# Performance work log

Measured on AMD Instinct MI355X. Metric: run time of the kernel, lower is better.

The kernel has to match this reference:

```python
import jax, jax.numpy as jnp
import numpy as np

EMBED_DIM = 1024
NUM_HEADS = 16
NUM_KV_HEADS = 4
HEAD_DIM = 64
WINDOW_SIZE = 32
TOKENS_PER_FRAME = 64
BASE_T, BASE_D, BASE_B = 10000.0, 100.0, 100.0


def apply_3d_rope(x, pos_t, pos_d, pos_b):
    # x: (B, S, H, D); pos_*: (S,) int
    D = x.shape[-1]
    half = D // 2
    dim_idx = jnp.arange(half, dtype=jnp.float32)
    inv_freq = 1.0 / (BASE_T ** (2.0 * dim_idx / D))  # (half,)
    ang = (pos_t.astype(jnp.float32)[:, None] * inv_freq
           + pos_d.astype(jnp.float32)[:, None] * inv_freq * (BASE_T / BASE_D)
           + pos_b.astype(jnp.float32)[:, None] * inv_freq * (BASE_T / BASE_B))  # (S, half)
    cos = jnp.cos(ang)[None, :, None, :]
    sin = jnp.sin(ang)[None, :, None, :]
    x1 = x[..., 0::2]
    x2 = x[..., 1::2]
    y1 = x1 * cos - x2 * sin
    y2 = x1 * sin + x2 * cos
    return jnp.stack([y1, y2], axis=-1).reshape(x.shape)


def setup_inputs() -> dict:
    key = jax.random.key(0)
    ks = jax.random.split(key, 8)
    B, Sn, Lp = 1, 1024, 4096
    hidden_states = jax.random.normal(ks[0], (B, Sn, EMBED_DIM), dtype=jnp.float32)
    past_k = jax.random.normal(ks[1], (B, NUM_KV_HEADS, Lp, HEAD_DIM), dtype=jnp.float32)
    past_v = jax.random.normal(ks[2], (B, NUM_KV_HEADS, Lp, HEAD_DIM), dtype=jnp.float32)
    wq = jax.random.normal(ks[3], (EMBED_DIM, NUM_HEADS * HEAD_DIM), dtype=jnp.float32) * 0.02
    wk = jax.random.normal(ks[4], (EMBED_DIM, NUM_KV_HEADS * HEAD_DIM), dtype=jnp.float32) * 0.02
    wv = jax.random.normal(ks[5], (EMBED_DIM, NUM_KV_HEADS * HEAD_DIM), dtype=jnp.float32) * 0.02
    wo = jax.random.normal(ks[6], (NUM_HEADS * HEAD_DIM, EMBED_DIM), dtype=jnp.float32) * 0.02
    # frame-time positions: tokens_per_frame tokens share a frame time; past frames 0..63, new frames 64..79
    past_idx = jnp.arange(Lp, dtype=jnp.int32)
    new_idx = jnp.arange(Sn, dtype=jnp.int32)
    past_t = past_idx // TOKENS_PER_FRAME
    new_t = new_idx // TOKENS_PER_FRAME + Lp // TOKENS_PER_FRAME
    # 8x8 depth-by-bearing patch grid within each frame
    past_d = (past_idx % TOKENS_PER_FRAME) // 8
    past_b = past_idx % 8
    new_d = (new_idx % TOKENS_PER_FRAME) // 8
    new_b = new_idx % 8
    return dict(hidden_states=hidden_states, past_k=past_k, past_v=past_v,
                wq=wq, wk=wk, wv=wv, wo=wo,
                new_t=new_t, new_d=new_d, new_b=new_b,
                past_t=past_t, past_d=past_d, past_b=past_b)


def reference(hidden_states, past_k, past_v, wq, wk, wv, wo,
              new_t, new_d, new_b, past_t, past_d, past_b):
    B, Sn, _ = hidden_states.shape
    Lp = past_t.shape[0]
    Q = (hidden_states @ wq).reshape(B, Sn, NUM_HEADS, HEAD_DIM)
    Kn = (hidden_states @ wk).reshape(B, Sn, NUM_KV_HEADS, HEAD_DIM)
    Vn = (hidden_states @ wv).reshape(B, Sn, NUM_KV_HEADS, HEAD_DIM)
    Q = apply_3d_rope(Q, new_t, new_d, new_b)
    Kn = apply_3d_rope(Kn, new_t, new_d, new_b)
    Q = Q.transpose(0, 2, 1, 3)   # (B, H, Sn, D)
    Kn = Kn.transpose(0, 2, 1, 3)  # (B, KVH, Sn, D)
    Vn = Vn.transpose(0, 2, 1, 3)
    # Sliding-window truncation on frame time: torch does searchsorted + slice
    # (drop past keys with time < min_time). Masking those keys to -inf is
    # mathematically identical and jit-friendly (static shapes).
    min_time = new_t.max() - (WINDOW_SIZE - 1)
    past_keep = past_t >= min_time                                    # (Lp,)
    valid = jnp.concatenate([past_keep, jnp.ones((Sn,), dtype=bool)])  # (Lp+Sn,)
    pos_t = jnp.concatenate([past_t, new_t])
    K = jnp.concatenate([past_k, Kn], axis=2)  # (B, KVH, Lp+Sn, D)
    V = jnp.concatenate([past_v, Vn], axis=2)
    rep = NUM_HEADS // NUM_KV_HEADS
    K = jnp.repeat(K, rep, axis=1)  # (B, H, L, D) -- repeat_interleave semantics
    V = jnp.repeat(V, rep, axis=1)
    scores = jnp.einsum('bhqd,bhkd->bhqk', Q, K) / jnp.sqrt(jnp.float32(HEAD_DIM))
    mask = (pos_t[None, :] <= new_t[:, None]) & valid[None, :]  # (Sn, L) frame-causal + window
    scores = jnp.where(mask[None, None], scores, jnp.float32(-jnp.inf))
    attn = jax.nn.softmax(scores, axis=-1)
    attn = jnp.nan_to_num(attn)  # fully-masked rows -> 0 (matches torch nan_to_num)
    out = jnp.einsum('bhqk,bhkd->bhqd', attn, V)
    out = out.transpose(0, 2, 1, 3).reshape(B, Sn, NUM_HEADS * HEAD_DIM)
    out = out @ wo
    return out, Kn, Vn
```

## Files before the change

kernel.cpp:

```cpp
#include <hip/hip_runtime.h>
#include <math.h>

#define EMBED 1024
#define NH 16
#define NKV 4
#define HD 64
#define SN 1024
#define LP 4096
#define WIN 32

#define FREQ_C 0.4152410118609203f

typedef float floatx4 __attribute__((ext_vector_type(4)));
typedef __bf16 bf16x8 __attribute__((ext_vector_type(8)));

__global__ __launch_bounds__(256) void prep_kernel(
    const float* __restrict__ hidden, const float* __restrict__ wq,
    const float* __restrict__ wk, const float* __restrict__ wv,
    const float* __restrict__ wo,
    __bf16* __restrict__ hidb, __bf16* __restrict__ wqT,
    __bf16* __restrict__ wkT, __bf16* __restrict__ wvT,
    __bf16* __restrict__ woT)
{
    const int jb = blockIdx.x, tid = threadIdx.x;
    if (jb >= 640) {
        const size_t base = (size_t)(jb - 640) * 4096 + (size_t)tid * 16;
        float4 f0 = *(const float4*)(hidden + base);
        float4 f1 = *(const float4*)(hidden + base + 4);
        float4 f2 = *(const float4*)(hidden + base + 8);
        float4 f3 = *(const float4*)(hidden + base + 12);
        bf16x8 o0, o1;
        o0[0] = (__bf16)f0.x; o0[1] = (__bf16)f0.y;
        o0[2] = (__bf16)f0.z; o0[3] = (__bf16)f0.w;
        o0[4] = (__bf16)f1.x; o0[5] = (__bf16)f1.y;
        o0[6] = (__bf16)f1.z; o0[7] = (__bf16)f1.w;
        o1[0] = (__bf16)f2.x; o1[1] = (__bf16)f2.y;
        o1[2] = (__bf16)f2.z; o1[3] = (__bf16)f2.w;
        o1[4] = (__bf16)f3.x; o1[5] = (__bf16)f3.y;
        o1[6] = (__bf16)f3.z; o1[7] = (__bf16)f3.w;
        *(bf16x8*)(hidb + base) = o0;
        *(bf16x8*)(hidb + base + 8) = o1;
        return;
    }
    const float* src; __bf16* dst; int N, tk, tn;
    if (jb < 256)      { src = wq; dst = wqT; N = 1024; tk = jb >> 4;         tn = jb & 15; }
    else if (jb < 320) { src = wk; dst = wkT; N = 256;  tk = (jb - 256) >> 2; tn = (jb - 256) & 3; }
    else if (jb < 384) { src = wv; dst = wvT; N = 256;  tk = (jb - 320) >> 2; tn = (jb - 320) & 3; }
    else               { src = wo; dst = woT; N = 1024; tk = (jb - 384) >> 4; tn = (jb - 384) & 15; }

    __shared__ float T[64][65];
    {
        const int r = tid >> 2, c0 = (tid & 3) * 16;
        const float* sp = src + (size_t)(tk * 64 + r) * N + tn * 64 + c0;
        float4 v0 = *(const float4*)(sp + 0);
        float4 v1 = *(const float4*)(sp + 4);
        float4 v2 = *(const float4*)(sp + 8);
        float4 v3 = *(const float4*)(sp + 12);
        *(float4*)&T[r][c0 + 0] = v0;
        *(float4*)&T[r][c0 + 4] = v1;
        *(float4*)&T[r][c0 + 8] = v2;
        *(float4*)&T[r][c0 + 12] = v3;
    }
    __syncthreads();
    {
        const int n = tid >> 2, k0 = (tid & 3) * 16;
        bf16x8 o0, o1;
#pragma unroll
        for (int j = 0; j < 8; j++) {
            o0[j] = (__bf16)T[k0 + j][n];
            o1[j] = (__bf16)T[k0 + 8 + j][n];
        }
        __bf16* dp = dst + (size_t)(tn * 64 + n) * 1024 + tk * 64 + k0;
        *(bf16x8*)dp = o0;
        *(bf16x8*)(dp + 8) = o1;
    }
}

__global__ __launch_bounds__(256) void qkv_mfma_kernel(
    const __bf16* __restrict__ hidb, const __bf16* __restrict__ wqT,
    const __bf16* __restrict__ wkT, const __bf16* __restrict__ wvT,
    const int* __restrict__ new_t, const int* __restrict__ new_d,
    const int* __restrict__ new_b,
    __bf16* __restrict__ qws, float* __restrict__ knp, float* __restrict__ vnp)
{
    __shared__ __bf16 ASh[32][72];
    __shared__ __bf16 BSh[64][72];

    const int tid = threadIdx.x;
    const int lane = tid & 63, w = tid >> 6;
    const int g = lane >> 4, c = lane & 15;
    const int bx = blockIdx.x, by = blockIdx.y;

    int mode, cbase;
    const __bf16* W;
    if (bx < 16)      { mode = 0; W = wqT; cbase = bx * 64; }
    else if (bx < 20) { mode = 1; W = wkT; cbase = (bx - 16) * 64; }
    else              { mode = 2; W = wvT; cbase = (bx - 20) * 64; }

    const int arow = tid >> 3, ak = (tid & 7) * 8;
    const __bf16* Ap = hidb + (size_t)(by * 32 + arow) * EMBED + ak;
    const int bn = tid & 63, bk0 = (tid >> 6) * 16;
    const __bf16* Bp = W + (size_t)(cbase + bn) * 1024 + bk0;

    floatx4 acc[2] = {floatx4(0.f), floatx4(0.f)};

    bf16x8 a0 = *(const bf16x8*)(Ap);
    bf16x8 b0 = *(const bf16x8*)(Bp);
    bf16x8 b1 = *(const bf16x8*)(Bp + 8);

    const int mt = (w & 1) * 16;
    const int nt0 = (w >> 1) * 2;

    for (int k0 = 0; k0 < EMBED; k0 += 64) {
        __syncthreads();
        *(bf16x8*)&ASh[arow][ak] = a0;
        *(bf16x8*)&BSh[bn][bk0] = b0;
        *(bf16x8*)&BSh[bn][bk0 + 8] = b1;
        __syncthreads();
        if (k0 + 64 < EMBED) {
            a0 = *(const bf16x8*)(Ap + k0 + 64);
            b0 = *(const bf16x8*)(Bp + k0 + 64);
            b1 = *(const bf16x8*)(Bp + k0 + 72);
        }
        bf16x8 af0 = *(const bf16x8*)&ASh[mt + c][g * 8];
        bf16x8 af1 = *(const bf16x8*)&ASh[mt + c][32 + g * 8];
#pragma unroll
        for (int t = 0; t < 2; t++) {
            const int tn = nt0 + t;
            bf16x8 bf0 = *(const bf16x8*)&BSh[tn * 16 + c][g * 8];
            bf16x8 bf1 = *(const bf16x8*)&BSh[tn * 16 + c][32 + g * 8];
            acc[t] = __builtin_amdgcn_mfma_f32_16x16x32_bf16(af0, bf0, acc[t], 0, 0, 0);
            acc[t] = __builtin_amdgcn_mfma_f32_16x16x32_bf16(af1, bf1, acc[t], 0, 0, 0);
        }
    }

    const int m0 = mt + g * 4;
    if (mode == 2) {
        const int kvh = bx - 20;
#pragma unroll
        for (int r = 0; r < 4; r++) {
            const int token = by * 32 + m0 + r;
#pragma unroll
            for (int t = 0; t < 2; t++)
                vnp[((size_t)kvh * SN + token) * HD + (nt0 + t) * 16 + c] = acc[t][r];
        }
    } else {
        float fr[2];
#pragma unroll
        for (int t = 0; t < 2; t++) {
            const int d = (cbase + (nt0 + t) * 16 + c) & 63;
            fr[t] = exp2f(-FREQ_C * (float)(d >> 1));
        }
        const int par = c & 1;
#pragma unroll
        for (int r = 0; r < 4; r++) {
            const int token = by * 32 + m0 + r;
            const float ft = (float)new_t[token];
            const float fdb = (float)(new_d[token] + new_b[token]);
#pragma unroll
            for (int t = 0; t < 2; t++) {
                const float ang = ft * fr[t] + fdb * (fr[t] * 100.0f);
                float sv, cv;
                sincosf(ang, &sv, &cv);
                const float x = acc[t][r];
                const float xp = __shfl_xor(x, 1, 64);
                const float y = par ? (xp * sv + x * cv) : (x * cv - xp * sv);
                const int col = cbase + (nt0 + t) * 16 + c;
                if (mode == 0) {
                    qws[(size_t)token * EMBED + col] = (__bf16)y;
                } else {
                    const int kvh = bx - 16;
                    knp[((size_t)kvh * SN + token) * HD + (col & 63)] = y;
                }
            }
        }
    }
}

__global__ __launch_bounds__(256) void out_mfma_kernel(
    const __bf16* __restrict__ ctxb, const __bf16* __restrict__ woT,
    float* __restrict__ C)
{
    __shared__ __bf16 ASh[32][72];
    __shared__ __bf16 BSh[64][72];

    const int tid = threadIdx.x;
    const int lane = tid & 63, w = tid >> 6;
    const int g = lane >> 4, c = lane & 15;
    const int bx = blockIdx.x, by = blockIdx.y;

    const int arow = tid >> 3, ak = (tid & 7) * 8;
    const __bf16* Ap = ctxb + (size_t)(by * 32 + arow) * EMBED + ak;
    const int bn = tid & 63, bk0 = (tid >> 6) * 16;
    const __bf16* Bp = woT + (size_t)(bx * 64 + bn) * 1024 + bk0;

    floatx4 acc[2] = {floatx4(0.f), floatx4(0.f)};

    bf16x8 a0 = *(const bf16x8*)(Ap);
    bf16x8 b0 = *(const bf16x8*)(Bp);
    bf16x8 b1 = *(const bf16x8*)(Bp + 8);

    const int mt = (w & 1) * 16;
    const int nt0 = (w >> 1) * 2;

    for (int k0 = 0; k0 < EMBED; k0 += 64) {
        __syncthreads();
        *(bf16x8*)&ASh[arow][ak] = a0;
        *(bf16x8*)&BSh[bn][bk0] = b0;
        *(bf16x8*)&BSh[bn][bk0 + 8] = b1;
        __syncthreads();
        if (k0 + 64 < EMBED) {
            a0 = *(const bf16x8*)(Ap + k0 + 64);
            b0 = *(const bf16x8*)(Bp + k0 + 64);
            b1 = *(const bf16x8*)(Bp + k0 + 72);
        }
        bf16x8 af0 = *(const bf16x8*)&ASh[mt + c][g * 8];
        bf16x8 af1 = *(const bf16x8*)&ASh[mt + c][32 + g * 8];
#pragma unroll
        for (int t = 0; t < 2; t++) {
            const int tn = nt0 + t;
            bf16x8 bf0 = *(const bf16x8*)&BSh[tn * 16 + c][g * 8];
            bf16x8 bf1 = *(const bf16x8*)&BSh[tn * 16 + c][32 + g * 8];
            acc[t] = __builtin_amdgcn_mfma_f32_16x16x32_bf16(af0, bf0, acc[t], 0, 0, 0);
            acc[t] = __builtin_amdgcn_mfma_f32_16x16x32_bf16(af1, bf1, acc[t], 0, 0, 0);
        }
    }

    const int m0 = mt + g * 4;
#pragma unroll
    for (int r = 0; r < 4; r++) {
        const int row = by * 32 + m0 + r;
#pragma unroll
        for (int t = 0; t < 2; t++)
            C[(size_t)row * EMBED + bx * 64 + (nt0 + t) * 16 + c] = acc[t][r];
    }
}

#define PREFETCH_CHUNK(CI)                                                     \
    {                                                                          \
        const int base_ = (myStart + (CI)) << 6;                               \
        const int gk_ = base_ + skk;                                           \
        if (gk_ < Nk) {                                                        \
            const float* kp_ = (gk_ < nPast)                                   \
                ? past_k + ((size_t)(kvh * LP + p0 + gk_)) * HD + sd0          \
                : knp + ((size_t)(kvh * SN + (gk_ - nPast))) * HD + sd0;       \
            kb0 = *(const float4*)(kp_ + 0);                                   \
            kb1 = *(const float4*)(kp_ + 4);                                   \
            kb2 = *(const float4*)(kp_ + 8);                                   \
            kb3 = *(const float4*)(kp_ + 12);                                  \
        } else {                                                               \
            kb0 = kb1 = kb2 = kb3 = make_float4(0.f, 0.f, 0.f, 0.f);           \
        }                                                                      \
        const int gv0_ = base_ + 2 * kp2;                                      \
        if (gv0_ < Nk) {                                                       \
            const float* vp_ = (gv0_ < nPast)                                  \
                ? past_v + ((size_t)(kvh * LP + p0 + gv0_)) * HD + vdb         \
                : vnp + ((size_t)(kvh * SN + (gv0_ - nPast))) * HD + vdb;      \
            vb00 = *(const float4*)(vp_ + 0);                                  \
            vb01 = *(const float4*)(vp_ + 4);                                  \
        } else {                                                               \
            vb00 = vb01 = make_float4(0.f, 0.f, 0.f, 0.f);                     \
        }                                                                      \
        const int gv1_ = gv0_ + 1;                                             \
        if (gv1_ < Nk) {                                                       \
            const float* vp_ = (gv1_ < nPast)                                  \
                ? past_v + ((size_t)(kvh * LP + p0 + gv1_)) * HD + vdb         \
                : vnp + ((size_t)(kvh * SN + (gv1_ - nPast))) * HD + vdb;      \
            vb10 = *(const float4*)(vp_ + 0);                                  \
            vb11 = *(const float4*)(vp_ + 4);                                  \
        } else {                                                               \
            vb10 = vb11 = make_float4(0.f, 0.f, 0.f, 0.f);                     \
        }                                                                      \
        if (tid < 64) {                                                        \
            const int g2_ = base_ + tid;                                       \
            ptreg = (g2_ < Nk)                                                 \
                ? ((g2_ < nPast) ? past_t[p0 + g2_] : new_t[g2_ - nPast])      \
                : 0x7fffffff;                                                  \
        }                                                                      \
    }

__global__ __launch_bounds__(256) void attn_kernel(
    const __bf16* __restrict__ qws, const float* __restrict__ past_k,
    const float* __restrict__ past_v, const float* __restrict__ knp,
    const float* __restrict__ vnp, const int* __restrict__ new_t,
    const int* __restrict__ past_t, float* __restrict__ opart,
    float* __restrict__ lpart)
{
    __shared__ __bf16 KS[64][72];
    __shared__ __bf16 VS[64][72];
    __shared__ __bf16 PS[4][64][72];
    __shared__ float MSK[64];

    const int tid = threadIdx.x;
    const int i = blockIdx.x;
    const int kvh = i & 3;
    const int sidx = (i >> 2) & 7;
    const int f = i >> 5;

    const int lane = tid & 63, w = tid >> 6;
    const int g = lane >> 4, c = lane & 15;
    const int h = kvh * 4 + w;

    const int tmax = new_t[SN - 1];
    const int min_time = tmax - (WIN - 1);
    const int qtf = new_t[f * 64];

    int lo = 0, hi = LP;
    while (lo < hi) {
        int mid = (lo + hi) >> 1;
        if (past_t[mid] >= min_time) hi = mid; else lo = mid + 1;
    }
    const int p0 = lo;
    const int nPast = LP - p0;
    const int Nk = nPast + (f + 1) * 64;

    const int nch = (Nk + 63) >> 6;
    const int qch = nch >> 3, rem = nch & 7;
    const int myCount = qch + (sidx < rem ? 1 : 0);
    const int myStart = sidx * qch + (sidx < rem ? sidx : rem);

    bf16x8 aQ[4][2];
#pragma unroll
    for (int qt = 0; qt < 4; qt++) {
        const __bf16* qp = qws + (size_t)(f * 64 + qt * 16 + c) * EMBED + h * HD + g * 8;
        aQ[qt][0] = *(const bf16x8*)(qp);
        aQ[qt][1] = *(const bf16x8*)(qp + 32);
    }

    floatx4 oacc[4][4];
#pragma unroll
    for (int qt = 0; qt < 4; qt++)
#pragma unroll
        for (int t = 0; t < 4; t++) oacc[qt][t] = floatx4(0.f);
    floatx4 lacc[4] = {floatx4(0.f), floatx4(0.f), floatx4(0.f), floatx4(0.f)};
    bf16x8 bOnes;
#pragma unroll
    for (int j = 0; j < 8; j++) bOnes[j] = (__bf16)1.0f;

    const float scale = 0.125f;

    const int skk = tid >> 2, sd0 = (tid & 3) * 16;
    const int kp2 = tid & 31, vdb = (tid >> 5) * 8;

    float4 kb0, kb1, kb2, kb3;
    float4 vb00, vb01, vb10, vb11;
    int ptreg = 0x7fffffff;

    if (myCount > 0) PREFETCH_CHUNK(0);

    for (int chi = 0; chi < myCount; ++chi) {
        __syncthreads();

        {
            bf16x8 t0, t1;
            t0[0] = (__bf16)kb0.x; t0[1] = (__bf16)kb0.y;
            t0[2] = (__bf16)kb0.z; t0[3] = (__bf16)kb0.w;
            t0[4] = (__bf16)kb1.x; t0[5] = (__bf16)kb1.y;
            t0[6] = (__bf16)kb1.z; t0[7] = (__bf16)kb1.w;
            t1[0] = (__bf16)kb2.x; t1[1] = (__bf16)kb2.y;
            t1[2] = (__bf16)kb2.z; t1[3] = (__bf16)kb2.w;
            t1[4] = (__bf16)kb3.x; t1[5] = (__bf16)kb3.y;
            t1[6] = (__bf16)kb3.z; t1[7] = (__bf16)kb3.w;
            *(bf16x8*)&KS[skk][sd0] = t0;
            *(bf16x8*)&KS[skk][sd0 + 8] = t1;
        }
        {
            float e0[8] = {vb00.x, vb00.y, vb00.z, vb00.w,
                           vb01.x, vb01.y, vb01.z, vb01.w};
            float e1[8] = {vb10.x, vb10.y, vb10.z, vb10.w,
                           vb11.x, vb11.y, vb11.z, vb11.w};
#pragma unroll
            for (int j = 0; j < 8; j++) {
                union { __bf16 b[2]; unsigned u; } pk;
                pk.b[0] = (__bf16)e0[j];
                pk.b[1] = (__bf16)e1[j];
                *(unsigned*)&VS[vdb + j][2 * kp2] = pk.u;
            }
        }
        if (tid < 64) {
            const int g2 = ((myStart + chi) << 6) + tid;
            const bool ok = (ptreg <= qtf) && ((g2 >= nPast) || (ptreg >= min_time));
            MSK[tid] = ok ? 0.f : -1e30f;
        }
        __syncthreads();

        if (chi + 1 < myCount) PREFETCH_CHUNK(chi + 1);

        bf16x8 kf[4][2];
#pragma unroll
        for (int kt = 0; kt < 4; kt++) {
            kf[kt][0] = *(const bf16x8*)&KS[kt * 16 + c][g * 8];
            kf[kt][1] = *(const bf16x8*)&KS[kt * 16 + c][32 + g * 8];
        }
        float mk[4];
#pragma unroll
        for (int kt = 0; kt < 4; kt++) mk[kt] = MSK[kt * 16 + c];

#pragma unroll
        for (int qt = 0; qt < 4; qt++) {
            floatx4 sacc[4];
#pragma unroll
            for (int kt = 0; kt < 4; kt++) {
                sacc[kt] = floatx4(0.f);
                sacc[kt] = __builtin_amdgcn_mfma_f32_16x16x32_bf16(aQ[qt][0], kf[kt][0], sacc[kt], 0, 0, 0);
                sacc[kt] = __builtin_amdgcn_mfma_f32_16x16x32_bf16(aQ[qt][1], kf[kt][1], sacc[kt], 0, 0, 0);
            }
#pragma unroll
            for (int r = 0; r < 4; r++)
#pragma unroll
                for (int kt = 0; kt < 4; kt++)
                    PS[w][qt * 16 + g * 4 + r][kt * 16 + c] =
                        (__bf16)__expf(sacc[kt][r] * scale + mk[kt]);
        }

#pragma unroll
        for (int s = 0; s < 2; s++) {
            bf16x8 af[4];
#pragma unroll
            for (int qt = 0; qt < 4; qt++)
                af[qt] = *(const bf16x8*)&PS[w][qt * 16 + c][s * 32 + g * 8];
#pragma unroll
            for (int qt = 0; qt < 4; qt++)
                lacc[qt] = __builtin_amdgcn_mfma_f32_16x16x32_bf16(af[qt], bOnes, lacc[qt], 0, 0, 0);
#pragma unroll
            for (int t = 0; t < 4; t++) {
                bf16x8 vf = *(const bf16x8*)&VS[t * 16 + c][s * 32 + g * 8];
#pragma unroll
                for (int qt = 0; qt < 4; qt++)
                    oacc[qt][t] = __builtin_amdgcn_mfma_f32_16x16x32_bf16(af[qt], vf, oacc[qt][t], 0, 0, 0);
            }
        }
    }

    float* Op = opart + ((size_t)(f * 16 + h) * 8 + sidx) * 4096;
    float* lp = lpart + ((size_t)(f * 16 + h) * 8 + sidx) * 64;
#pragma unroll
    for (int qt = 0; qt < 4; qt++) {
#pragma unroll
        for (int r = 0; r < 4; r++) {
            const int q = qt * 16 + g * 4 + r;
#pragma unroll
            for (int t = 0; t < 4; t++)
                Op[(size_t)q * 64 + t * 16 + c] = oacc[qt][t][r];
            if (c == 0) lp[q] = lacc[qt][r];
        }
    }
}

__global__ __launch_bounds__(256) void attn_merge_kernel(
    const float* __restrict__ opart, const float* __restrict__ lpart,
    __bf16* __restrict__ ctxb)
{
    const int f = blockIdx.x, h = blockIdx.y;
    const int tid = threadIdx.x;
    const int q = tid >> 2, d0 = (tid & 3) * 16;
    const size_t fh = (size_t)(f * 16 + h);

    float l = 0.f;
#pragma unroll
    for (int s = 0; s < 8; s++) l += lpart[(fh * 8 + s) * 64 + q];
    const float inv = (l > 0.f) ? (1.f / l) : 0.f;

    float o[16] = {};
#pragma unroll
    for (int s = 0; s < 8; s++) {
        const float* Os = opart + (fh * 8 + s) * 4096 + (size_t)q * 64 + d0;
#pragma unroll
        for (int v = 0; v < 4; v++) {
            float4 ov = *(const float4*)(Os + v * 4);
            o[v * 4 + 0] += ov.x;
            o[v * 4 + 1] += ov.y;
            o[v * 4 + 2] += ov.z;
            o[v * 4 + 3] += ov.w;
        }
    }
    bf16x8 o0, o1;
#pragma unroll
    for (int j = 0; j < 8; j++) {
        o0[j] = (__bf16)(o[j] * inv);
        o1[j] = (__bf16)(o[8 + j] * inv);
    }
    __bf16* cp = ctxb + (size_t)(f * 64 + q) * EMBED + h * HD + d0;
    *(bf16x8*)cp = o0;
    *(bf16x8*)(cp + 8) = o1;
}

extern "C" void kernel_launch(void* const* d_in, const int* in_sizes, int n_in,
                              void* d_out, int out_size, void* d_ws, size_t ws_size,
                              hipStream_t stream) {
    const float* hidden = (const float*)d_in[0];
    const float* past_k = (const float*)d_in[1];
    const float* past_v = (const float*)d_in[2];
    const float* wq     = (const float*)d_in[3];
    const float* wk     = (const float*)d_in[4];
    const float* wv     = (const float*)d_in[5];
    const float* wo     = (const float*)d_in[6];
    const int* new_t    = (const int*)d_in[7];
    const int* new_d    = (const int*)d_in[8];
    const int* new_b    = (const int*)d_in[9];
    const int* past_t   = (const int*)d_in[10];

    float* out = (float*)d_out;
    float* knp = out + SN * EMBED;
    float* vnp = knp + NKV * SN * HD;

    float* lpart = (float*)d_ws;
    float* opart = lpart + (size_t)16 * 16 * 8 * 64;
    __bf16* qws  = (__bf16*)(opart + (size_t)16 * 16 * 8 * 4096);
    __bf16* hidb = qws + (size_t)SN * EMBED;
    __bf16* wqT  = hidb + (size_t)SN * EMBED;
    __bf16* wkT  = wqT + (size_t)1024 * 1024;
    __bf16* wvT  = wkT + (size_t)256 * 1024;
    __bf16* woT  = wvT + (size_t)256 * 1024;
    __bf16* ctxb = woT + (size_t)1024 * 1024;

    prep_kernel<<<dim3(896), 256, 0, stream>>>(
        hidden, wq, wk, wv, wo, hidb, wqT, wkT, wvT, woT);
    qkv_mfma_kernel<<<dim3(24, 32), 256, 0, stream>>>(
        hidb, wqT, wkT, wvT, new_t, new_d, new_b, qws, knp, vnp);
    attn_kernel<<<dim3(512), 256, 0, stream>>>(
        qws, past_k, past_v, knp, vnp, new_t, past_t, opart, lpart);
    attn_merge_kernel<<<dim3(16, 16), 256, 0, stream>>>(opart, lpart, ctxb);
    out_mfma_kernel<<<dim3(16, 32), 256, 0, stream>>>(ctxb, woT, out);
}
```

Before: 147.2 us.

## Pre-pack windowed K/V into bf16 with transposed V before attention

Adds a kvpack kernel that converts the windowed past and new K/V to bf16 once per KV head, storing V transposed and the key frame times compactly. The attention kernel then streams half-width bf16 tiles with plain vector stores into shared memory, which removes the per-block fp32 loads, conversions and scattered V transpose that were repeated across query frames. The P tile is halved by processing query tiles in pairs, K fragments are reloaded from LDS instead of held in registers, and launch bounds ask for 3 blocks per CU. The costs are an extra kernel launch, an extra pass over K/V through global memory, and more LDS reads per chunk.

```diff
diff --git a/kernel.cpp b/kernel.cpp
--- a/kernel.cpp
+++ b/kernel.cpp
@@ -8,6 +8,7 @@
 #define SN 1024
 #define LP 4096
 #define WIN 32
+#define KMAX 5184
 
 #define FREQ_C 0.4152410118609203f
 
@@ -177,6 +178,87 @@
     }
 }
 
+__global__ __launch_bounds__(256) void kvpack_kernel(
+    const float* __restrict__ past_k, const float* __restrict__ past_v,
+    const float* __restrict__ knp, const float* __restrict__ vnp,
+    const int* __restrict__ past_t, const int* __restrict__ new_t,
+    __bf16* __restrict__ Kb, __bf16* __restrict__ VTb, int* __restrict__ ptb)
+{
+    const int kvh = blockIdx.x & 3;
+    const int chunk = blockIdx.x >> 2;
+    const int tid = threadIdx.x;
+
+    const int tmax = new_t[SN - 1];
+    const int min_time = tmax - (WIN - 1);
+    int lo = 0, hi = LP;
+    while (lo < hi) {
+        int mid = (lo + hi) >> 1;
+        if (past_t[mid] >= min_time) hi = mid; else lo = mid + 1;
+    }
+    const int p0 = lo;
+    const int nPast = LP - p0;
+    const int NkT = nPast + SN;
+    const int base = chunk * 64;
+    if (base >= NkT) return;
+
+    __shared__ float T[64][65];
+
+    {
+        const int kk = tid >> 2, d0 = (tid & 3) * 16;
+        const int gk = base + kk;
+        if (gk < NkT) {
+            const size_t koff = (gk < nPast)
+                ? ((size_t)(kvh * LP + p0 + gk)) * HD + d0
+                : ((size_t)(kvh * SN + (gk - nPast))) * HD + d0;
+            const float* kp = (gk < nPast) ? past_k + koff : knp + koff;
+            const float* vp = (gk < nPast) ? past_v + koff : vnp + koff;
+            float4 k0 = *(const float4*)(kp + 0);
+            float4 k1 = *(const float4*)(kp + 4);
+            float4 k2 = *(const float4*)(kp + 8);
+            float4 k3 = *(const float4*)(kp + 12);
+            bf16x8 t0, t1;
+            t0[0] = (__bf16)k0.x; t0[1] = (__bf16)k0.y;
+            t0[2] = (__bf16)k0.z; t0[3] = (__bf16)k0.w;
+            t0[4] = (__bf16)k1.x; t0[5] = (__bf16)k1.y;
+            t0[6] = (__bf16)k1.z; t0[7] = (__bf16)k1.w;
+            t1[0] = (__bf16)k2.x; t1[1] = (__bf16)k2.y;
+            t1[2] = (__bf16)k2.z; t1[3] = (__bf16)k2.w;
+            t1[4] = (__bf16)k3.x; t1[5] = (__bf16)k3.y;
+            t1[6] = (__bf16)k3.z; t1[7] = (__bf16)k3.w;
+            __bf16* kd = Kb + ((size_t)kvh * KMAX + gk) * HD + d0;
+            *(bf16x8*)kd = t0;
+            *(bf16x8*)(kd + 8) = t1;
+            *(float4*)&T[kk][d0 + 0] = *(const float4*)(vp + 0);
+            *(float4*)&T[kk][d0 + 4] = *(const float4*)(vp + 4);
+            *(float4*)&T[kk][d0 + 8] = *(const float4*)(vp + 8);
+            *(float4*)&T[kk][d0 + 12] = *(const float4*)(vp + 12);
+        } else {
+            *(float4*)&T[kk][d0 + 0] = make_float4(0.f, 0.f, 0.f, 0.f);
+            *(float4*)&T[kk][d0 + 4] = make_float4(0.f, 0.f, 0.f, 0.f);
+            *(float4*)&T[kk][d0 + 8] = make_float4(0.f, 0.f, 0.f, 0.f);
+            *(float4*)&T[kk][d0 + 12] = make_float4(0.f, 0.f, 0.f, 0.f);
+        }
+        if (kvh == 0 && tid < 64) {
+            const int g2 = base + tid;
+            if (g2 < NkT)
+                ptb[g2] = (g2 < nPast) ? past_t[p0 + g2] : new_t[g2 - nPast];
+        }
+    }
+    __syncthreads();
+    {
+        const int d = tid >> 2, kb = (tid & 3) * 16;
+        bf16x8 o0, o1;
+#pragma unroll
+        for (int j = 0; j < 8; j++) {
+            o0[j] = (__bf16)T[kb + j][d];
+            o1[j] = (__bf16)T[kb + 8 + j][d];
+        }
+        __bf16* vd = VTb + ((size_t)kvh * HD + d) * KMAX + base + kb;
+        *(bf16x8*)vd = o0;
+        *(bf16x8*)(vd + 8) = o1;
+    }
+}
+
 __global__ __launch_bounds__(256) void out_mfma_kernel(
     const __bf16* __restrict__ ctxb, const __bf16* __restrict__ woT,
     float* __restrict__ C)
@@ -239,56 +321,24 @@
 #define PREFETCH_CHUNK(CI)                                                     \
     {                                                                          \
         const int base_ = (myStart + (CI)) << 6;                               \
-        const int gk_ = base_ + skk;                                           \
-        if (gk_ < Nk) {                                                        \
-            const float* kp_ = (gk_ < nPast)                                   \
-                ? past_k + ((size_t)(kvh * LP + p0 + gk_)) * HD + sd0          \
-                : knp + ((size_t)(kvh * SN + (gk_ - nPast))) * HD + sd0;       \
-            kb0 = *(const float4*)(kp_ + 0);                                   \
-            kb1 = *(const float4*)(kp_ + 4);                                   \
-            kb2 = *(const float4*)(kp_ + 8);                                   \
-            kb3 = *(const float4*)(kp_ + 12);                                  \
-        } else {                                                               \
-            kb0 = kb1 = kb2 = kb3 = make_float4(0.f, 0.f, 0.f, 0.f);           \
-        }                                                                      \
-        const int gv0_ = base_ + 2 * kp2;                                      \
-        if (gv0_ < Nk) {                                                       \
-            const float* vp_ = (gv0_ < nPast)                                  \
-                ? past_v + ((size_t)(kvh * LP + p0 + gv0_)) * HD + vdb         \
-                : vnp + ((size_t)(kvh * SN + (gv0_ - nPast))) * HD + vdb;      \
-            vb00 = *(const float4*)(vp_ + 0);                                  \
-            vb01 = *(const float4*)(vp_ + 4);                                  \
-        } else {                                                               \
-            vb00 = vb01 = make_float4(0.f, 0.f, 0.f, 0.f);                     \
-        }                                                                      \
-        const int gv1_ = gv0_ + 1;                                             \
-        if (gv1_ < Nk) {                                                       \
-            const float* vp_ = (gv1_ < nPast)                                  \
-                ? past_v + ((size_t)(kvh * LP + p0 + gv1_)) * HD + vdb         \
-                : vnp + ((size_t)(kvh * SN + (gv1_ - nPast))) * HD + vdb;      \
-            vb10 = *(const float4*)(vp_ + 0);                                  \
-            vb11 = *(const float4*)(vp_ + 4);                                  \
-        } else {                                                               \
-            vb10 = vb11 = make_float4(0.f, 0.f, 0.f, 0.f);                     \
-        }                                                                      \
-        if (tid < 64) {                                                        \
-            const int g2_ = base_ + tid;                                       \
-            ptreg = (g2_ < Nk)                                                 \
-                ? ((g2_ < nPast) ? past_t[p0 + g2_] : new_t[g2_ - nPast])      \
-                : 0x7fffffff;                                                  \
-        }                                                                      \
-    }
-
-__global__ __launch_bounds__(256) void attn_kernel(
-    const __bf16* __restrict__ qws, const float* __restrict__ past_k,
-    const float* __restrict__ past_v, const float* __restrict__ knp,
-    const float* __restrict__ vnp, const int* __restrict__ new_t,
-    const int* __restrict__ past_t, float* __restrict__ opart,
-    float* __restrict__ lpart)
+        const __bf16* kp_ = Kb + ((size_t)kvh * KMAX + base_ + skk) * HD + sd0;\
+        kb0 = *(const bf16x8*)kp_;                                             \
+        kb1 = *(const bf16x8*)(kp_ + 8);                                       \
+        const __bf16* vp_ = VTb + ((size_t)kvh * HD + vd) * KMAX + base_ + vkb;\
+        vb0 = *(const bf16x8*)vp_;                                             \
+        vb1 = *(const bf16x8*)(vp_ + 8);                                       \
+        if (tid < 64) ptreg = ptb[base_ + tid];                                \
+    }
+
+__global__ __launch_bounds__(256, 3) void attn_kernel(
+    const __bf16* __restrict__ qws, const __bf16* __restrict__ Kb,
+    const __bf16* __restrict__ VTb, const int* __restrict__ ptb,
+    const int* __restrict__ new_t, const int* __restrict__ past_t,
+    float* __restrict__ opart, float* __restrict__ lpart)
 {
     __shared__ __bf16 KS[64][72];
     __shared__ __bf16 VS[64][72];
-    __shared__ __bf16 PS[4][64][72];
+    __shared__ __bf16 PS[4][32][72];
     __shared__ float MSK[64];
 
     const int tid = threadIdx.x;
@@ -310,8 +360,7 @@
         int mid = (lo + hi) >> 1;
         if (past_t[mid] >= min_time) hi = mid; else lo = mid + 1;
     }
-    const int p0 = lo;
-    const int nPast = LP - p0;
+    const int nPast = LP - lo;
     const int Nk = nPast + (f + 1) * 64;
 
     const int nch = (Nk + 63) >> 6;
@@ -340,10 +389,9 @@
     const float scale = 0.125f;
 
     const int skk = tid >> 2, sd0 = (tid & 3) * 16;
-    const int kp2 = tid & 31, vdb = (tid >> 5) * 8;
-
-    float4 kb0, kb1, kb2, kb3;
-    float4 vb00, vb01, vb10, vb11;
+    const int vd = tid >> 2, vkb = (tid & 3) * 16;
+
+    bf16x8 kb0, kb1, vb0, vb1;
     int ptreg = 0x7fffffff;
 
     if (myCount > 0) PREFETCH_CHUNK(0);
@@ -351,83 +399,55 @@
     for (int chi = 0; chi < myCount; ++chi) {
         __syncthreads();
 
-        {
-            bf16x8 t0, t1;
-            t0[0] = (__bf16)kb0.x; t0[1] = (__bf16)kb0.y;
-            t0[2] = (__bf16)kb0.z; t0[3] = (__bf16)kb0.w;
-            t0[4] = (__bf16)kb1.x; t0[5] = (__bf16)kb1.y;
-            t0[6] = (__bf16)kb1.z; t0[7] = (__bf16)kb1.w;
-            t1[0] = (__bf16)kb2.x; t1[1] = (__bf16)kb2.y;
-            t1[2] = (__bf16)kb2.z; t1[3] = (__bf16)kb2.w;
-            t1[4] = (__bf16)kb3.x; t1[5] = (__bf16)kb3.y;
-            t1[6] = (__bf16)kb3.z; t1[7] = (__bf16)kb3.w;
-            *(bf16x8*)&KS[skk][sd0] = t0;
-            *(bf16x8*)&KS[skk][sd0 + 8] = t1;
-        }
-        {
-            float e0[8] = {vb00.x, vb00.y, vb00.z, vb00.w,
-                           vb01.x, vb01.y, vb01.z, vb01.w};
-            float e1[8] = {vb10.x, vb10.y, vb10.z, vb10.w,
-                           vb11.x, vb11.y, vb11.z, vb11.w};
-#pragma unroll
-            for (int j = 0; j < 8; j++) {
-                union { __bf16 b[2]; unsigned u; } pk;
-                pk.b[0] = (__bf16)e0[j];
-                pk.b[1] = (__bf16)e1[j];
-                *(unsigned*)&VS[vdb + j][2 * kp2] = pk.u;
-            }
-        }
+        *(bf16x8*)&KS[skk][sd0] = kb0;
+        *(bf16x8*)&KS[skk][sd0 + 8] = kb1;
+        *(bf16x8*)&VS[vd][vkb] = vb0;
+        *(bf16x8*)&VS[vd][vkb + 8] = vb1;
         if (tid < 64) {
             const int g2 = ((myStart + chi) << 6) + tid;
-            const bool ok = (ptreg <= qtf) && ((g2 >= nPast) || (ptreg >= min_time));
-            MSK[tid] = ok ? 0.f : -1e30f;
+            MSK[tid] = ((g2 < Nk) && (ptreg <= qtf)) ? 0.f : -1e30f;
         }
         __syncthreads();
 
         if (chi + 1 < myCount) PREFETCH_CHUNK(chi + 1);
 
-        bf16x8 kf[4][2];
-#pragma unroll
-        for (int kt = 0; kt < 4; kt++) {
-            kf[kt][0] = *(const bf16x8*)&KS[kt * 16 + c][g * 8];
-            kf[kt][1] = *(const bf16x8*)&KS[kt * 16 + c][32 + g * 8];
-        }
-        float mk[4];
-#pragma unroll
-        for (int kt = 0; kt < 4; kt++) mk[kt] = MSK[kt * 16 + c];
-
-#pragma unroll
-        for (int qt = 0; qt < 4; qt++) {
-            floatx4 sacc[4];
-#pragma unroll
-            for (int kt = 0; kt < 4; kt++) {
-                sacc[kt] = floatx4(0.f);
-                sacc[kt] = __builtin_amdgcn_mfma_f32_16x16x32_bf16(aQ[qt][0], kf[kt][0], sacc[kt], 0, 0, 0);
-                sacc[kt] = __builtin_amdgcn_mfma_f32_16x16x32_bf16(aQ[qt][1], kf[kt][1], sacc[kt], 0, 0, 0);
+#pragma unroll
+        for (int qp = 0; qp < 2; qp++) {
+#pragma unroll
+            for (int u = 0; u < 2; u++) {
+                const int qt = qp * 2 + u;
+                floatx4 sacc[4];
+#pragma unroll
+                for (int kt = 0; kt < 4; kt++) {
+                    bf16x8 k0 = *(const bf16x8*)&KS[kt * 16 + c][g * 8];
+                    bf16x8 k1 = *(const bf16x8*)&KS[kt * 16 + c][32 + g * 8];
+                    sacc[kt] = floatx4(0.f);
+                    sacc[kt] = __builtin_amdgcn_mfma_f32_16x16x32_bf16(aQ[qt][0], k0, sacc[kt], 0, 0, 0);
+                    sacc[kt] = __builtin_amdgcn_mfma_f32_16x16x32_bf16(aQ[qt][1], k1, sacc[kt], 0, 0, 0);
+                }
+#pragma unroll
+                for (int r = 0; r < 4; r++)
+#pragma unroll
+                    for (int kt = 0; kt < 4; kt++)
+                        PS[w][u * 16 + g * 4 + r][kt * 16 + c] =
+                            (__bf16)__expf(sacc[kt][r] * scale + MSK[kt * 16 + c]);
             }
 #pragma unroll
-            for (int r = 0; r < 4; r++)
-#pragma unroll
-                for (int kt = 0; kt < 4; kt++)
-                    PS[w][qt * 16 + g * 4 + r][kt * 16 + c] =
-                        (__bf16)__expf(sacc[kt][r] * scale + mk[kt]);
-        }
-
-#pragma unroll
-        for (int s = 0; s < 2; s++) {
-            bf16x8 af[4];
-#pragma unroll
-            for (int qt = 0; qt < 4; qt++)
-                af[qt] = *(const bf16x8*)&PS[w][qt * 16 + c][s * 32 + g * 8];
-#pragma unroll
-            for (int qt = 0; qt < 4; qt++)
-                lacc[qt] = __builtin_amdgcn_mfma_f32_16x16x32_bf16(af[qt], bOnes, lacc[qt], 0, 0, 0);
-#pragma unroll
-            for (int t = 0; t < 4; t++) {
-                bf16x8 vf = *(const bf16x8*)&VS[t * 16 + c][s * 32 + g * 8];
-#pragma unroll
-                for (int qt = 0; qt < 4; qt++)
-                    oacc[qt][t] = __builtin_amdgcn_mfma_f32_16x16x32_bf16(af[qt], vf, oacc[qt][t], 0, 0, 0);
+            for (int s = 0; s < 2; s++) {
+                bf16x8 af[2];
+#pragma unroll
+                for (int u = 0; u < 2; u++)
+                    af[u] = *(const bf16x8*)&PS[w][u * 16 + c][s * 32 + g * 8];
+#pragma unroll
+                for (int u = 0; u < 2; u++)
+                    lacc[qp * 2 + u] = __builtin_amdgcn_mfma_f32_16x16x32_bf16(af[u], bOnes, lacc[qp * 2 + u], 0, 0, 0);
+#pragma unroll
+                for (int t = 0; t < 4; t++) {
+                    bf16x8 vf = *(const bf16x8*)&VS[t * 16 + c][s * 32 + g * 8];
+#pragma unroll
+                    for (int u = 0; u < 2; u++)
+                        oacc[qp * 2 + u][t] = __builtin_amdgcn_mfma_f32_16x16x32_bf16(af[u], vf, oacc[qp * 2 + u][t], 0, 0, 0);
+                }
             }
         }
     }
@@ -513,13 +533,18 @@
     __bf16* wvT  = wkT + (size_t)256 * 1024;
     __bf16* woT  = wvT + (size_t)256 * 1024;
     __bf16* ctxb = woT + (size_t)1024 * 1024;
+    __bf16* Kb   = ctxb + (size_t)SN * EMBED;
+    __bf16* VTb  = Kb + (size_t)NKV * KMAX * HD;
+    int*    ptb  = (int*)(VTb + (size_t)NKV * HD * KMAX);
 
     prep_kernel<<<dim3(896), 256, 0, stream>>>(
         hidden, wq, wk, wv, wo, hidb, wqT, wkT, wvT, woT);
     qkv_mfma_kernel<<<dim3(24, 32), 256, 0, stream>>>(
         hidb, wqT, wkT, wvT, new_t, new_d, new_b, qws, knp, vnp);
+    kvpack_kernel<<<dim3(4 * (KMAX / 64)), 256, 0, stream>>>(
+        past_k, past_v, knp, vnp, past_t, new_t, Kb, VTb, ptb);
     attn_kernel<<<dim3(512), 256, 0, stream>>>(
-        qws, past_k, past_v, knp, vnp, new_t, past_t, opart, lpart);
+        qws, Kb, VTb, ptb, new_t, past_t, opart, lpart);
     attn_merge_kernel<<<dim3(16, 16), 256, 0, stream>>>(opart, lpart, ctxb);
     out_mfma_kernel<<<dim3(16, 32), 256, 0, stream>>>(ctxb, woT, out);
 }
```

Result: slower. 158.4 us (+7.6%).
